# Optimization experiments

Measured on AMD Instinct MI355X. Metric: run time of the kernel, lower is better.

## Reference

```python
import jax, jax.numpy as jnp
import numpy as np

N = 50000      # nodes
E = 800000     # edges (before self loops)
F_IN = 256     # input features
C = 64         # out_channels per head
H = 4          # heads
NC = 3         # num_class


def setup_inputs() -> dict:
    key = jax.random.key(0)
    ks = jax.random.split(key, 11)
    s = 0.1
    return {
        "x": jax.random.normal(ks[0], (N, F_IN), jnp.float32),
        "edge_index": jax.random.randint(ks[1], (2, E), 0, N, dtype=jnp.int64),
        # conv1: in=F_IN -> H*C, concat
        "W1": jax.random.normal(ks[2], (H * C, F_IN), jnp.float32) * s,
        "as1": jax.random.normal(ks[3], (H, C), jnp.float32) * s,
        "ad1": jax.random.normal(ks[4], (H, C), jnp.float32) * s,
        "b1": jnp.zeros((H * C,), jnp.float32),
        # conv2: in=H*C -> H*C, concat
        "W2": jax.random.normal(ks[5], (H * C, H * C), jnp.float32) * s,
        "as2": jax.random.normal(ks[6], (H, C), jnp.float32) * s,
        "ad2": jax.random.normal(ks[7], (H, C), jnp.float32) * s,
        "b2": jnp.zeros((H * C,), jnp.float32),
        # conv3: in=H*C -> NC, heads averaged (concat=False)
        "W3": jax.random.normal(ks[8], (H * NC, H * C), jnp.float32) * s,
        "as3": jax.random.normal(ks[9], (H, NC), jnp.float32) * s,
        "ad3": jax.random.normal(ks[10], (H, NC), jnp.float32) * s,
        "b3": jnp.zeros((NC,), jnp.float32),
    }


def _gat_conv(x, src, dst, W, a_src, a_dst, b, concat):
    # x: [N,F]; src/dst: [E'] (self loops included); W: [H*C, F]; a_*: [H,C]
    n = x.shape[0]
    h_, c_ = a_src.shape
    h = (x @ W.T).reshape(n, h_, c_)                       # [N,H,C]
    alpha_src = (h * a_src[None]).sum(-1)                  # [N,H]
    alpha_dst = (h * a_dst[None]).sum(-1)                  # [N,H]
    e = jax.nn.leaky_relu(alpha_src[src] + alpha_dst[dst], 0.2)  # [E',H]
    # segment softmax over destination-node neighborhoods
    m = jax.ops.segment_max(e, dst, num_segments=n)        # [N,H]
    ex = jnp.exp(e - m[dst])
    den = jax.ops.segment_sum(ex, dst, num_segments=n)     # [N,H]
    alpha = ex / den[dst]                                  # [E',H]
    out = jax.ops.segment_sum(h[src] * alpha[:, :, None], dst, num_segments=n)  # [N,H,C]
    if concat:
        return out.reshape(n, h_ * c_) + b
    return out.mean(axis=1) + b


def reference(x, edge_index, W1, as1, ad1, b1, W2, as2, ad2, b2, W3, as3, ad3, b3):
    n = x.shape[0]
    loop = jnp.arange(n, dtype=edge_index.dtype)
    src = jnp.concatenate([edge_index[0], loop])  # add_self_loops=True
    dst = jnp.concatenate([edge_index[1], loop])
    x = jax.nn.elu(_gat_conv(x, src, dst, W1, as1, ad1, b1, True))
    x = jax.nn.elu(_gat_conv(x, src, dst, W2, as2, ad2, b2, True))
    x = jax.nn.elu(_gat_conv(x, src, dst, W3, as3, ad3, b3, False))
    return x
```

## Files before the change

### kernel.cpp

```cpp
#include <hip/hip_runtime.h>
#include <hip/hip_fp16.h>
#include <cstdint>
#include <cstddef>

#define NNODES 50000
#define NEDGES 800000
#define E2 (NEDGES + NNODES)
#define HC 256

typedef __attribute__((ext_vector_type(8))) short short8v;
typedef __attribute__((ext_vector_type(4))) float f32x4;
typedef const __attribute__((address_space(1))) void* gas_t;
typedef __attribute__((address_space(3))) void* las_t;


__global__ void zero_int(int* __restrict__ p, int n) {
    int i = blockIdx.x * 256 + threadIdx.x;
    if (i < n) p[i] = 0;
}

__global__ void count_deg(const int* __restrict__ ei, int* __restrict__ deg) {
    int i = blockIdx.x * 256 + threadIdx.x;
    if (i >= E2) return;
    int d = (i < NEDGES) ? ei[NEDGES + i] : (i - NEDGES);
    atomicAdd(&deg[d], 1);
}

__global__ void scan1(const int* __restrict__ deg, int* __restrict__ rp, int* __restrict__ bs) {
    __shared__ int s[256];
    int t = threadIdx.x, i = blockIdx.x * 256 + t;
    int v = (i < NNODES) ? deg[i] : 0;
    s[t] = v;
    __syncthreads();
    for (int o = 1; o < 256; o <<= 1) {
        int add = (t >= o) ? s[t - o] : 0;
        __syncthreads();
        s[t] += add;
        __syncthreads();
    }
    if (i < NNODES) rp[i] = s[t] - v;
    if (t == 255) bs[blockIdx.x] = s[255];
}

__global__ void scan2(int* __restrict__ bs, int nb) {
    __shared__ int s[256];
    int t = threadIdx.x;
    int v = (t < nb) ? bs[t] : 0;
    s[t] = v;
    __syncthreads();
    for (int o = 1; o < 256; o <<= 1) {
        int add = (t >= o) ? s[t - o] : 0;
        __syncthreads();
        s[t] += add;
        __syncthreads();
    }
    bs[t] = s[t] - v;
}

__global__ void scan3(int* __restrict__ rp, const int* __restrict__ bs, int* __restrict__ cnt) {
    int i = blockIdx.x * 256 + threadIdx.x;
    if (i < NNODES) {
        int v = rp[i] + bs[blockIdx.x];
        rp[i] = v;
        cnt[i] = v;
    }
    if (i == 0) rp[NNODES] = E2;
}

__global__ void fill_csr(const int* __restrict__ ei, int* __restrict__ cnt, int* __restrict__ csr) {
    int i = blockIdx.x * 256 + threadIdx.x;
    if (i >= E2) return;
    int s, d;
    if (i < NEDGES) { s = ei[i]; d = ei[NEDGES + i]; }
    else            { s = d = i - NEDGES; }
    int pos = atomicAdd(&cnt[d], 1);
    csr[pos] = s;
}


__device__ __forceinline__ unsigned short f2bf(float f) {
    uint32_t u = __float_as_uint(f);
    uint32_t r = (u + 0x7FFFu + ((u >> 16) & 1u)) >> 16;
    return (unsigned short)r;
}
__device__ __forceinline__ float bf2f(unsigned short h) {
    return __uint_as_float(((uint32_t)h) << 16);
}

__global__ void split_bf16(const float* __restrict__ in, unsigned short* __restrict__ hi,
                           unsigned short* __restrict__ lo, int n4) {
    int i = blockIdx.x * 256 + threadIdx.x;
    if (i >= n4) return;
    float4 v = ((const float4*)in)[i];
    unsigned short h0 = f2bf(v.x), h1 = f2bf(v.y), h2 = f2bf(v.z), h3 = f2bf(v.w);
    unsigned short l0 = f2bf(v.x - bf2f(h0));
    unsigned short l1 = f2bf(v.y - bf2f(h1));
    unsigned short l2 = f2bf(v.z - bf2f(h2));
    unsigned short l3 = f2bf(v.w - bf2f(h3));
    uint2 hp, lp;
    hp.x = (uint32_t)h0 | ((uint32_t)h1 << 16);
    hp.y = (uint32_t)h2 | ((uint32_t)h3 << 16);
    lp.x = (uint32_t)l0 | ((uint32_t)l1 << 16);
    lp.y = (uint32_t)l2 | ((uint32_t)l3 << 16);
    *(uint2*)(hi + 4 * (size_t)i) = hp;
    *(uint2*)(lo + 4 * (size_t)i) = lp;
}


__global__ __launch_bounds__(256, 2) void gemm_mfma(
    const unsigned short* __restrict__ Ah, const unsigned short* __restrict__ Al,
    const unsigned short* __restrict__ Wh, const unsigned short* __restrict__ Wl,
    _Float16* __restrict__ out16, int M) {
    __shared__ unsigned short sAh[2][128][32], sAl[2][128][32], sWh[2][128][32], sWl[2][128][32];
    const int t = threadIdx.x;
    const int m0 = blockIdx.x * 128, n0 = blockIdx.y * 128;
    const int lane = t & 63, w = t >> 6;
    const int wr = w >> 1, wc = w & 1;
    const int fr = lane & 15, fg = lane >> 4;

    const int u0 = (w * 2) * 64 + lane, u1 = (w * 2 + 1) * 64 + lane;
    const int row0 = u0 >> 2, cb0 = (u0 & 3) * 8;
    const int row1 = u1 >> 2, cb1 = (u1 & 3) * 8;
    int gra0 = m0 + row0; gra0 = gra0 < M ? gra0 : M - 1;
    int gra1 = m0 + row1; gra1 = gra1 < M ? gra1 : M - 1;
    const int grw0 = n0 + row0, grw1 = n0 + row1;

    auto stage = [&](int b, int kc) {
        __builtin_amdgcn_global_load_lds((gas_t)(Ah + (size_t)gra0 * HC + kc + cb0), (las_t)&sAh[b][row0][cb0], 16, 0, 0);
        __builtin_amdgcn_global_load_lds((gas_t)(Ah + (size_t)gra1 * HC + kc + cb1), (las_t)&sAh[b][row1][cb1], 16, 0, 0);
        __builtin_amdgcn_global_load_lds((gas_t)(Al + (size_t)gra0 * HC + kc + cb0), (las_t)&sAl[b][row0][cb0], 16, 0, 0);
        __builtin_amdgcn_global_load_lds((gas_t)(Al + (size_t)gra1 * HC + kc + cb1), (las_t)&sAl[b][row1][cb1], 16, 0, 0);
        __builtin_amdgcn_global_load_lds((gas_t)(Wh + (size_t)grw0 * HC + kc + cb0), (las_t)&sWh[b][row0][cb0], 16, 0, 0);
        __builtin_amdgcn_global_load_lds((gas_t)(Wh + (size_t)grw1 * HC + kc + cb1), (las_t)&sWh[b][row1][cb1], 16, 0, 0);
        __builtin_amdgcn_global_load_lds((gas_t)(Wl + (size_t)grw0 * HC + kc + cb0), (las_t)&sWl[b][row0][cb0], 16, 0, 0);
        __builtin_amdgcn_global_load_lds((gas_t)(Wl + (size_t)grw1 * HC + kc + cb1), (las_t)&sWl[b][row1][cb1], 16, 0, 0);
    };

    f32x4 acc[4][4];
#pragma unroll
    for (int mi = 0; mi < 4; mi++)
#pragma unroll
        for (int ni = 0; ni < 4; ni++) acc[mi][ni] = (f32x4){0.f, 0.f, 0.f, 0.f};

    auto compute = [&](int b) {
        short8v ah[4], al[4], bh[4], bl[4];
#pragma unroll
        for (int i = 0; i < 4; i++) {
            ah[i] = *(const short8v*)&sAh[b][wr * 64 + i * 16 + fr][fg * 8];
            al[i] = *(const short8v*)&sAl[b][wr * 64 + i * 16 + fr][fg * 8];
            bh[i] = *(const short8v*)&sWh[b][wc * 64 + i * 16 + fr][fg * 8];
            bl[i] = *(const short8v*)&sWl[b][wc * 64 + i * 16 + fr][fg * 8];
        }
#pragma unroll
        for (int mi = 0; mi < 4; mi++)
#pragma unroll
            for (int ni = 0; ni < 4; ni++) {
                acc[mi][ni] = __builtin_amdgcn_mfma_f32_16x16x32_bf16(ah[mi], bh[ni], acc[mi][ni], 0, 0, 0);
                acc[mi][ni] = __builtin_amdgcn_mfma_f32_16x16x32_bf16(ah[mi], bl[ni], acc[mi][ni], 0, 0, 0);
                acc[mi][ni] = __builtin_amdgcn_mfma_f32_16x16x32_bf16(al[mi], bh[ni], acc[mi][ni], 0, 0, 0);
            }
    };

    stage(0, 0);
    __syncthreads();
#pragma unroll
    for (int kt = 0; kt < 7; kt++) {
        stage((kt + 1) & 1, (kt + 1) * 32);
        compute(kt & 1);
        __syncthreads();
    }
    compute(1);

#pragma unroll
    for (int mi = 0; mi < 4; mi++) {
#pragma unroll
        for (int r = 0; r < 4; r++) {
            int gr = m0 + wr * 64 + mi * 16 + fg * 4 + r;
            if (gr < M) {
#pragma unroll
                for (int ni = 0; ni < 4; ni++) {
                    out16[(size_t)gr * HC + n0 + wc * 64 + ni * 16 + fr] = (_Float16)acc[mi][ni][r];
                }
            }
        }
    }
}


__global__ void alpha_hc(const _Float16* __restrict__ h16, const float* __restrict__ a_s,
                         const float* __restrict__ a_d, float* __restrict__ asrc,
                         float* __restrict__ adst) {
    int n = blockIdx.x * 4 + (threadIdx.x >> 6);
    int lane = threadIdx.x & 63;
    uint2 raw = *(const uint2*)(h16 + (size_t)n * HC + lane * 4);
    __half2 p0 = *(__half2*)&raw.x;
    __half2 p1 = *(__half2*)&raw.y;
    float h0 = __low2float(p0), h1 = __high2float(p0);
    float h2 = __low2float(p1), h3 = __high2float(p1);
    float4 s4 = *(const float4*)(a_s + lane * 4);
    float4 d4 = *(const float4*)(a_d + lane * 4);
    float ps = h0 * s4.x + h1 * s4.y + h2 * s4.z + h3 * s4.w;
    float pd = h0 * d4.x + h1 * d4.y + h2 * d4.z + h3 * d4.w;
#pragma unroll
    for (int o = 1; o < 16; o <<= 1) {
        ps += __shfl_xor(ps, o);
        pd += __shfl_xor(pd, o);
    }
    if ((lane & 15) == 0) {
        int hh = lane >> 4;
        asrc[n * 4 + hh] = ps;
        adst[n * 4 + hh] = pd;
    }
}


#define CHUNK 384
#define NPB 8

__global__ void aggregate_hc(const _Float16* __restrict__ h16, const float* __restrict__ asrc,
                             const float* __restrict__ adst, const int* __restrict__ rp,
                             const int* __restrict__ csr, const float* __restrict__ bias,
                             float* __restrict__ y, unsigned short* __restrict__ yh,
                             unsigned short* __restrict__ yl, int flags) {
    __shared__ int   sIdx[CHUNK];
    __shared__ int   sOff[NPB + 1];
    __shared__ float sE4[CHUNK][4];
    __shared__ float sM[NPB][4], sS[NPB][4];
    __shared__ float sAd[NPB][4];
    int n0 = blockIdx.x * NPB;
    int t = threadIdx.x;
    int r0 = rp[n0];
    int tot = rp[n0 + NPB] - r0;

    if (tot <= CHUNK) {
        if (t <= NPB) sOff[t] = rp[n0 + t] - r0;
        if (t >= 32 && t < 32 + NPB * 4) {
            int i = (t - 32) >> 2, hh = t & 3;
            sAd[i][hh] = adst[(n0 + i) * 4 + hh];
        }
        for (int j = t; j < tot; j += 256) sIdx[j] = csr[r0 + j];
        __syncthreads();

        int i = t >> 5, q = t & 31, hh = q >> 3, slot = q & 7;
        int js = sOff[i], je = sOff[i + 1];

        float adh = sAd[i][hh];
        float pm = -1e30f;
        for (int j = js + slot; j < je; j += 8) {
            int s = sIdx[j];
            float e = asrc[s * 4 + hh] + adh;
            e = e > 0.f ? e : 0.2f * e;
            sE4[j][hh] = e;
            pm = fmaxf(pm, e);
        }
#pragma unroll
        for (int o = 1; o < 8; o <<= 1) pm = fmaxf(pm, __shfl_xor(pm, o));
        if (slot == 0) sM[i][hh] = pm;
        __syncthreads();

        float mh = sM[i][hh];
        float ps = 0.f;
        for (int j = js + slot; j < je; j += 8) {
            float ex = __expf(sE4[j][hh] - mh);
            sE4[j][hh] = ex;
            ps += ex;
        }
#pragma unroll
        for (int o = 1; o < 8; o <<= 1) ps += __shfl_xor(ps, o);
        if (slot == 0) sS[i][hh] = ps;
        __syncthreads();

        float a[8];
#pragma unroll
        for (int k = 0; k < 8; k++) a[k] = 0.f;
        for (int j = js; j < je; j++) {
            int s = sIdx[j];
            float aw = sE4[j][hh];
            uint4 raw = *(const uint4*)(h16 + (size_t)s * HC + 8 * q);
            const _Float16* hv = reinterpret_cast<const _Float16*>(&raw);
#pragma unroll
            for (int k = 0; k < 8; k++) a[k] = fmaf((float)hv[k], aw, a[k]);
        }
        float inv = 1.f / sS[i][hh];
        size_t base = (size_t)(n0 + i) * HC + 8 * q;
#pragma unroll
        for (int k = 0; k < 8; k++) {
            float outv = a[k] * inv + bias[8 * q + k];
            outv = outv > 0.f ? outv : expm1f(outv);
            if (flags & 1) y[base + k] = outv;
            if (flags & 2) {
                unsigned short hi = f2bf(outv);
                yh[base + k] = hi;
                yl[base + k] = f2bf(outv - bf2f(hi));
            }
        }
    } else {
        for (int i = 0; i < NPB; i++) {
            int n = n0 + i;
            int rr0 = rp[n], deg = rp[n + 1] - rr0;
            int w = t >> 6, l = t & 63;
            float ad = adst[n * 4 + w];
            int hoff = (w << 6) + l;
            const _Float16* hp = h16 + hoff;
            float m = -1e30f;
            for (int j = l; j < deg; j += 64) {
                int s = csr[rr0 + j];
                float e = asrc[s * 4 + w] + ad;
                e = e > 0.f ? e : 0.2f * e;
                m = fmaxf(m, e);
            }
#pragma unroll
            for (int o = 32; o > 0; o >>= 1) m = fmaxf(m, __shfl_xor(m, o));
            float acc = 0.f, ssum = 0.f;
            for (int j = 0; j < deg; j++) {
                int s = csr[rr0 + j];
                float e = asrc[s * 4 + w] + ad;
                e = e > 0.f ? e : 0.2f * e;
                float aa = __expf(e - m);
                ssum += aa;
                acc = fmaf(aa, (float)hp[(size_t)s * HC], acc);
            }
            float outv = acc / ssum + bias[hoff];
            outv = outv > 0.f ? outv : expm1f(outv);
            size_t off = (size_t)n * HC + hoff;
            if (flags & 1) y[off] = outv;
            if (flags & 2) {
                unsigned short hi = f2bf(outv);
                yh[off] = hi;
                yl[off] = f2bf(outv - bf2f(hi));
            }
        }
    }
}


__global__ void gemm_small(const float* __restrict__ Y, const float* __restrict__ W3,
                           float* __restrict__ h3) {
    int idx = blockIdx.x * 256 + threadIdx.x;
    if (idx >= NNODES * 12) return;
    int n = idx / 12, o = idx - n * 12;
    const float4* xr = (const float4*)(Y + (size_t)n * HC);
    const float4* wr = (const float4*)(W3 + o * HC);
    float acc = 0.f;
#pragma unroll 8
    for (int k = 0; k < 64; k++) {
        float4 a = xr[k], b = wr[k];
        acc += a.x * b.x + a.y * b.y + a.z * b.z + a.w * b.w;
    }
    h3[idx] = acc;
}

__global__ void alpha3(const float* __restrict__ h3, const float* __restrict__ a_s,
                       const float* __restrict__ a_d, float* __restrict__ asrc,
                       float* __restrict__ adst) {
    int n = blockIdx.x * 256 + threadIdx.x;
    if (n >= NNODES) return;
    const float* hr = h3 + (size_t)n * 12;
    float s[4], d[4];
#pragma unroll
    for (int hh = 0; hh < 4; hh++) {
        s[hh] = hr[hh * 3] * a_s[hh * 3] + hr[hh * 3 + 1] * a_s[hh * 3 + 1] + hr[hh * 3 + 2] * a_s[hh * 3 + 2];
        d[hh] = hr[hh * 3] * a_d[hh * 3] + hr[hh * 3 + 1] * a_d[hh * 3 + 1] + hr[hh * 3 + 2] * a_d[hh * 3 + 2];
    }
    *(float4*)(asrc + n * 4) = make_float4(s[0], s[1], s[2], s[3]);
    *(float4*)(adst + n * 4) = make_float4(d[0], d[1], d[2], d[3]);
}

__global__ void aggregate3(const float* __restrict__ h3, const float* __restrict__ asrc,
                           const float* __restrict__ adst, const int* __restrict__ rp,
                           const int* __restrict__ csr, const float* __restrict__ b3,
                           float* __restrict__ out) {
    int n = blockIdx.x * 4 + (threadIdx.x >> 6);
    int l = threadIdx.x & 63;
    if (n >= NNODES) return;
    int r0 = rp[n], deg = rp[n + 1] - r0;
    float4 ad = *(const float4*)(adst + n * 4);

    float m0 = -1e30f, m1 = -1e30f, m2 = -1e30f, m3 = -1e30f;
    for (int j = l; j < deg; j += 64) {
        int s = csr[r0 + j];
        float4 a4 = *(const float4*)(asrc + s * 4);
        float e0 = a4.x + ad.x, e1 = a4.y + ad.y, e2 = a4.z + ad.z, e3 = a4.w + ad.w;
        e0 = e0 > 0.f ? e0 : 0.2f * e0;
        e1 = e1 > 0.f ? e1 : 0.2f * e1;
        e2 = e2 > 0.f ? e2 : 0.2f * e2;
        e3 = e3 > 0.f ? e3 : 0.2f * e3;
        m0 = fmaxf(m0, e0); m1 = fmaxf(m1, e1); m2 = fmaxf(m2, e2); m3 = fmaxf(m3, e3);
    }
    for (int o = 32; o > 0; o >>= 1) {
        m0 = fmaxf(m0, __shfl_xor(m0, o));
        m1 = fmaxf(m1, __shfl_xor(m1, o));
        m2 = fmaxf(m2, __shfl_xor(m2, o));
        m3 = fmaxf(m3, __shfl_xor(m3, o));
    }

    float acc[12];
#pragma unroll
    for (int k = 0; k < 12; k++) acc[k] = 0.f;
    float s0 = 0.f, s1 = 0.f, s2 = 0.f, s3 = 0.f;
    for (int j = l; j < deg; j += 64) {
        int s = csr[r0 + j];
        float4 a4 = *(const float4*)(asrc + s * 4);
        float e0 = a4.x + ad.x, e1 = a4.y + ad.y, e2 = a4.z + ad.z, e3 = a4.w + ad.w;
        e0 = e0 > 0.f ? e0 : 0.2f * e0;
        e1 = e1 > 0.f ? e1 : 0.2f * e1;
        e2 = e2 > 0.f ? e2 : 0.2f * e2;
        e3 = e3 > 0.f ? e3 : 0.2f * e3;
        float w0 = __expf(e0 - m0), w1 = __expf(e1 - m1), w2 = __expf(e2 - m2), w3 = __expf(e3 - m3);
        s0 += w0; s1 += w1; s2 += w2; s3 += w3;
        const float* hr = h3 + (size_t)s * 12;
#pragma unroll
        for (int c = 0; c < 3; c++) {
            acc[c]     += w0 * hr[c];
            acc[3 + c] += w1 * hr[3 + c];
            acc[6 + c] += w2 * hr[6 + c];
            acc[9 + c] += w3 * hr[9 + c];
        }
    }
    for (int o = 32; o > 0; o >>= 1) {
#pragma unroll
        for (int k = 0; k < 12; k++) acc[k] += __shfl_xor(acc[k], o);
        s0 += __shfl_xor(s0, o);
        s1 += __shfl_xor(s1, o);
        s2 += __shfl_xor(s2, o);
        s3 += __shfl_xor(s3, o);
    }
    if (l < 3) {
        float v = 0.25f * (acc[l] / s0 + acc[3 + l] / s1 + acc[6 + l] / s2 + acc[9 + l] / s3) + b3[l];
        v = v > 0.f ? v : expm1f(v);
        out[(size_t)n * 3 + l] = v;
    }
}


extern "C" void kernel_launch(void* const* d_in, const int* in_sizes, int n_in,
                              void* d_out, int out_size, void* d_ws, size_t ws_size,
                              hipStream_t stream) {
    (void)in_sizes; (void)n_in; (void)out_size; (void)ws_size;
    const float* x   = (const float*)d_in[0];
    const int*   ei  = (const int*)d_in[1];
    const float* W1  = (const float*)d_in[2];
    const float* as1 = (const float*)d_in[3];
    const float* ad1 = (const float*)d_in[4];
    const float* b1  = (const float*)d_in[5];
    const float* W2  = (const float*)d_in[6];
    const float* as2 = (const float*)d_in[7];
    const float* ad2 = (const float*)d_in[8];
    const float* b2  = (const float*)d_in[9];
    const float* W3  = (const float*)d_in[10];
    const float* as3 = (const float*)d_in[11];
    const float* ad3 = (const float*)d_in[12];
    const float* b3  = (const float*)d_in[13];
    float* out = (float*)d_out;

    uint8_t* p = (uint8_t*)d_ws;
    auto alloc = [&](size_t bytes) -> void* {
        void* r = (void*)p;
        p += (bytes + 255) & ~(size_t)255;
        return r;
    };
    float* bufY = (float*)alloc((size_t)NNODES * HC * 4);
    float* h3   = (float*)alloc((size_t)NNODES * 12 * 4);
    float* asrc = (float*)alloc((size_t)NNODES * 4 * 4);
    float* adst = (float*)alloc((size_t)NNODES * 4 * 4);
    int* deg    = (int*)alloc((size_t)NNODES * 4);
    int* rp     = (int*)alloc((size_t)(NNODES + 1) * 4);
    int* cnt    = (int*)alloc((size_t)NNODES * 4);
    int* csr    = (int*)alloc((size_t)E2 * 4);
    int* bsums  = (int*)alloc(256 * 4);
    unsigned short* xh  = (unsigned short*)alloc((size_t)NNODES * HC * 2);
    unsigned short* xl  = (unsigned short*)alloc((size_t)NNODES * HC * 2);
    unsigned short* w1h = (unsigned short*)alloc((size_t)HC * HC * 2);
    unsigned short* w1l = (unsigned short*)alloc((size_t)HC * HC * 2);
    unsigned short* w2h = (unsigned short*)alloc((size_t)HC * HC * 2);
    unsigned short* w2l = (unsigned short*)alloc((size_t)HC * HC * 2);
    _Float16* h16 = (_Float16*)alloc((size_t)NNODES * HC * 2);

    const int NB_N = (NNODES + 255) / 256;
    const int NB_E = (E2 + 255) / 256;
    const int N4_A = NNODES * HC / 4;
    const int N4_W = HC * HC / 4;

    zero_int<<<NB_N, 256, 0, stream>>>(deg, NNODES);
    count_deg<<<NB_E, 256, 0, stream>>>(ei, deg);
    scan1<<<NB_N, 256, 0, stream>>>(deg, rp, bsums);
    scan2<<<1, 256, 0, stream>>>(bsums, NB_N);
    scan3<<<NB_N, 256, 0, stream>>>(rp, bsums, cnt);
    fill_csr<<<NB_E, 256, 0, stream>>>(ei, cnt, csr);

    dim3 ggrid((NNODES + 127) / 128, 2);

    split_bf16<<<(N4_W + 255) / 256, 256, 0, stream>>>(W1, w1h, w1l, N4_W);
    split_bf16<<<(N4_A + 255) / 256, 256, 0, stream>>>(x, xh, xl, N4_A);
    gemm_mfma<<<ggrid, 256, 0, stream>>>(xh, xl, w1h, w1l, h16, NNODES);
    alpha_hc<<<NNODES / 4, 256, 0, stream>>>(h16, as1, ad1, asrc, adst);
    aggregate_hc<<<NNODES / NPB, 256, 0, stream>>>(h16, asrc, adst, rp, csr, b1, bufY, xh, xl, 2);

    split_bf16<<<(N4_W + 255) / 256, 256, 0, stream>>>(W2, w2h, w2l, N4_W);
    gemm_mfma<<<ggrid, 256, 0, stream>>>(xh, xl, w2h, w2l, h16, NNODES);
    alpha_hc<<<NNODES / 4, 256, 0, stream>>>(h16, as2, ad2, asrc, adst);
    aggregate_hc<<<NNODES / NPB, 256, 0, stream>>>(h16, asrc, adst, rp, csr, b2, bufY, xh, xl, 1);

    gemm_small<<<(NNODES * 12 + 255) / 256, 256, 0, stream>>>(bufY, W3, h3);
    alpha3<<<NB_N, 256, 0, stream>>>(h3, as3, ad3, asrc, adst);
    aggregate3<<<(NNODES + 3) / 4, 256, 0, stream>>>(h3, asrc, adst, rp, csr, b3, out);
}
```

Baseline: 640.0 us.

## Load GEMM weight fragments directly to registers and prefetch aggregation rows

The GEMM now reads the small weight matrix fragments straight from global memory into registers, with a one-step register prefetch, instead of staging them through LDS. This halves LDS usage and LDS traffic per block. In the aggregation loop the next neighbor's feature row is loaded one iteration ahead to hide gather latency. The cost is more VGPRs under the 2-wave launch bound, and the weight loads are uncoalesced and rely on the cache.

```diff
diff --git a/kernel.cpp b/kernel.cpp
--- a/kernel.cpp
+++ b/kernel.cpp
@@ -111,65 +111,81 @@
     const unsigned short* __restrict__ Ah, const unsigned short* __restrict__ Al,
     const unsigned short* __restrict__ Wh, const unsigned short* __restrict__ Wl,
     _Float16* __restrict__ out16, int M) {
-    __shared__ unsigned short sAh[2][128][32], sAl[2][128][32], sWh[2][128][32], sWl[2][128][32];
+    __shared__ unsigned short sAh[2][128][32], sAl[2][128][32];
     const int t = threadIdx.x;
     const int m0 = blockIdx.x * 128, n0 = blockIdx.y * 128;
     const int lane = t & 63, w = t >> 6;
     const int wr = w >> 1, wc = w & 1;
     const int fr = lane & 15, fg = lane >> 4;
 
-    const int u0 = (w * 2) * 64 + lane, u1 = (w * 2 + 1) * 64 + lane;
-    const int row0 = u0 >> 2, cb0 = (u0 & 3) * 8;
-    const int row1 = u1 >> 2, cb1 = (u1 & 3) * 8;
-    int gra0 = m0 + row0; gra0 = gra0 < M ? gra0 : M - 1;
-    int gra1 = m0 + row1; gra1 = gra1 < M ? gra1 : M - 1;
-    const int grw0 = n0 + row0, grw1 = n0 + row1;
-
-    auto stage = [&](int b, int kc) {
-        __builtin_amdgcn_global_load_lds((gas_t)(Ah + (size_t)gra0 * HC + kc + cb0), (las_t)&sAh[b][row0][cb0], 16, 0, 0);
-        __builtin_amdgcn_global_load_lds((gas_t)(Ah + (size_t)gra1 * HC + kc + cb1), (las_t)&sAh[b][row1][cb1], 16, 0, 0);
-        __builtin_amdgcn_global_load_lds((gas_t)(Al + (size_t)gra0 * HC + kc + cb0), (las_t)&sAl[b][row0][cb0], 16, 0, 0);
-        __builtin_amdgcn_global_load_lds((gas_t)(Al + (size_t)gra1 * HC + kc + cb1), (las_t)&sAl[b][row1][cb1], 16, 0, 0);
-        __builtin_amdgcn_global_load_lds((gas_t)(Wh + (size_t)grw0 * HC + kc + cb0), (las_t)&sWh[b][row0][cb0], 16, 0, 0);
-        __builtin_amdgcn_global_load_lds((gas_t)(Wh + (size_t)grw1 * HC + kc + cb1), (las_t)&sWh[b][row1][cb1], 16, 0, 0);
-        __builtin_amdgcn_global_load_lds((gas_t)(Wl + (size_t)grw0 * HC + kc + cb0), (las_t)&sWl[b][row0][cb0], 16, 0, 0);
-        __builtin_amdgcn_global_load_lds((gas_t)(Wl + (size_t)grw1 * HC + kc + cb1), (las_t)&sWl[b][row1][cb1], 16, 0, 0);
+    const int rowA0 = t >> 2, cbA0 = (t & 3) * 8;
+    const int rowA1 = rowA0 + 64, cbA1 = cbA0;
+    int gra0 = m0 + rowA0; gra0 = gra0 < M ? gra0 : M - 1;
+    int gra1 = m0 + rowA1; gra1 = gra1 < M ? gra1 : M - 1;
+
+    auto stageA = [&](int b, int kc) {
+        __builtin_amdgcn_global_load_lds((gas_t)(Ah + (size_t)gra0 * HC + kc + cbA0), (las_t)&sAh[b][rowA0][cbA0], 16, 0, 0);
+        __builtin_amdgcn_global_load_lds((gas_t)(Ah + (size_t)gra1 * HC + kc + cbA1), (las_t)&sAh[b][rowA1][cbA1], 16, 0, 0);
+        __builtin_amdgcn_global_load_lds((gas_t)(Al + (size_t)gra0 * HC + kc + cbA0), (las_t)&sAl[b][rowA0][cbA0], 16, 0, 0);
+        __builtin_amdgcn_global_load_lds((gas_t)(Al + (size_t)gra1 * HC + kc + cbA1), (las_t)&sAl[b][rowA1][cbA1], 16, 0, 0);
     };
 
+    const unsigned short* wph[4];
+    const unsigned short* wpl[4];
+#pragma unroll
+    for (int i = 0; i < 4; i++) {
+        int grw = n0 + wc * 64 + i * 16 + fr;
+        wph[i] = Wh + (size_t)grw * HC + fg * 8;
+        wpl[i] = Wl + (size_t)grw * HC + fg * 8;
+    }
+
     f32x4 acc[4][4];
 #pragma unroll
     for (int mi = 0; mi < 4; mi++)
 #pragma unroll
         for (int ni = 0; ni < 4; ni++) acc[mi][ni] = (f32x4){0.f, 0.f, 0.f, 0.f};
 
-    auto compute = [&](int b) {
-        short8v ah[4], al[4], bh[4], bl[4];
+    short8v bh[4], bl[4], bhn[4], bln[4];
+#pragma unroll
+    for (int i = 0; i < 4; i++) {
+        bh[i] = *(const short8v*)(wph[i]);
+        bl[i] = *(const short8v*)(wpl[i]);
+    }
+    stageA(0, 0);
+    __syncthreads();
+
+#pragma unroll
+    for (int kt = 0; kt < 8; kt++) {
+        const int kc = kt * 32;
+        if (kt < 7) {
+            stageA((kt + 1) & 1, kc + 32);
+#pragma unroll
+            for (int i = 0; i < 4; i++) {
+                bhn[i] = *(const short8v*)(wph[i] + kc + 32);
+                bln[i] = *(const short8v*)(wpl[i] + kc + 32);
+            }
+        }
+        const int b = kt & 1;
+        short8v a_h[4], a_l[4];
 #pragma unroll
         for (int i = 0; i < 4; i++) {
-            ah[i] = *(const short8v*)&sAh[b][wr * 64 + i * 16 + fr][fg * 8];
-            al[i] = *(const short8v*)&sAl[b][wr * 64 + i * 16 + fr][fg * 8];
-            bh[i] = *(const short8v*)&sWh[b][wc * 64 + i * 16 + fr][fg * 8];
-            bl[i] = *(const short8v*)&sWl[b][wc * 64 + i * 16 + fr][fg * 8];
+            a_h[i] = *(const short8v*)&sAh[b][wr * 64 + i * 16 + fr][fg * 8];
+            a_l[i] = *(const short8v*)&sAl[b][wr * 64 + i * 16 + fr][fg * 8];
         }
 #pragma unroll
         for (int mi = 0; mi < 4; mi++)
 #pragma unroll
             for (int ni = 0; ni < 4; ni++) {
-                acc[mi][ni] = __builtin_amdgcn_mfma_f32_16x16x32_bf16(ah[mi], bh[ni], acc[mi][ni], 0, 0, 0);
-                acc[mi][ni] = __builtin_amdgcn_mfma_f32_16x16x32_bf16(ah[mi], bl[ni], acc[mi][ni], 0, 0, 0);
-                acc[mi][ni] = __builtin_amdgcn_mfma_f32_16x16x32_bf16(al[mi], bh[ni], acc[mi][ni], 0, 0, 0);
-            }
-    };
-
-    stage(0, 0);
-    __syncthreads();
-#pragma unroll
-    for (int kt = 0; kt < 7; kt++) {
-        stage((kt + 1) & 1, (kt + 1) * 32);
-        compute(kt & 1);
-        __syncthreads();
-    }
-    compute(1);
+                acc[mi][ni] = __builtin_amdgcn_mfma_f32_16x16x32_bf16(a_h[mi], bh[ni], acc[mi][ni], 0, 0, 0);
+                acc[mi][ni] = __builtin_amdgcn_mfma_f32_16x16x32_bf16(a_h[mi], bl[ni], acc[mi][ni], 0, 0, 0);
+                acc[mi][ni] = __builtin_amdgcn_mfma_f32_16x16x32_bf16(a_l[mi], bh[ni], acc[mi][ni], 0, 0, 0);
+            }
+        if (kt < 7) {
+#pragma unroll
+            for (int i = 0; i < 4; i++) { bh[i] = bhn[i]; bl[i] = bln[i]; }
+        }
+        __syncthreads();
+    }
 
 #pragma unroll
     for (int mi = 0; mi < 4; mi++) {
@@ -273,13 +289,16 @@
         float a[8];
 #pragma unroll
         for (int k = 0; k < 8; k++) a[k] = 0.f;
-        for (int j = js; j < je; j++) {
-            int s = sIdx[j];
-            float aw = sE4[j][hh];
-            uint4 raw = *(const uint4*)(h16 + (size_t)s * HC + 8 * q);
-            const _Float16* hv = reinterpret_cast<const _Float16*>(&raw);
-#pragma unroll
-            for (int k = 0; k < 8; k++) a[k] = fmaf((float)hv[k], aw, a[k]);
+        if (js < je) {
+            uint4 raw = *(const uint4*)(h16 + (size_t)sIdx[js] * HC + 8 * q);
+            for (int j = js; j < je; j++) {
+                uint4 cur = raw;
+                if (j + 1 < je) raw = *(const uint4*)(h16 + (size_t)sIdx[j + 1] * HC + 8 * q);
+                float aw = sE4[j][hh];
+                const _Float16* hv = reinterpret_cast<const _Float16*>(&cur);
+#pragma unroll
+                for (int k = 0; k < 8; k++) a[k] = fmaf((float)hv[k], aw, a[k]);
+            }
         }
         float inv = 1.f / sS[i][hh];
         size_t base = (size_t)(n0 + i) * HC + 8 * q;
```

Measured after the change: 663.6 us. 1.04x slower.
